# Kernel tuning notes

Measured on AMD Instinct MI355X. Metric: run time of the kernel, lower is better.

## Reference

```python
import jax, jax.numpy as jnp
import numpy as np

B, T, D = 2, 2048, 2048
NH, HD, R = 16, 128, 64
CQ, CKV = 1536, 512
WINDOW, CHUNK = 512, 256
MIN_SCALE, MAX_SCALE = 0.5, 2.0
ROPE_BASE = 500000.0
EPS = 1e-6


def setup_inputs() -> dict:
    key = jax.random.key(0)
    ks = jax.random.split(key, 12)
    w = lambda k, shape: (jax.random.normal(k, shape, jnp.float32) * 0.02)
    return {
        "x": jax.random.normal(ks[0], (B, T, D), jnp.float32),
        "uncertainty": jax.random.uniform(ks[1], (B, T), jnp.float32),
        "Wq_down": w(ks[2], (D, CQ)),
        "q_norm_w": jnp.ones((CQ,), jnp.float32),
        "Wq_up": w(ks[3], (CQ, NH * HD)),
        "Wq_rope": w(ks[4], (CQ, NH * R)),
        "Wkv_down": w(ks[5], (D, CKV)),
        "kv_norm_w": jnp.ones((CKV,), jnp.float32),
        "Wk_up": w(ks[6], (CKV, NH * HD)),
        "Wv_up": w(ks[7], (CKV, NH * HD)),
        "Wk_rope": w(ks[8], (D, NH * R)),
        "Wout": w(ks[9], (NH * HD, D)),
        "Wgate": w(ks[10], (D, 1)),
        "bgate": jnp.zeros((1,), jnp.float32),
    }


def rms_norm(x, w):
    return x * jax.lax.rsqrt(jnp.mean(x * x, axis=-1, keepdims=True) + EPS) * w


def epe_cos_sin(positions, uncertainty):
    # freq_idx = arange(r//2)*2/r ; theta = base**(-freq_idx)
    half = R // 2
    freq_idx = jnp.arange(half, dtype=jnp.float32) * 2.0 / R
    theta = ROPE_BASE ** (-freq_idx)                                  # [half]
    scale = MIN_SCALE + jnp.clip(uncertainty, 0.0, 1.0) * (MAX_SCALE - MIN_SCALE)  # [B,T]
    freqs = positions[None, :, None].astype(jnp.float32) * theta[None, None, :] * scale[:, :, None]
    freqs = freqs[:, :, None, :]                                      # [B,T,1,half]
    return jnp.cos(freqs), jnp.sin(freqs)


def apply_rope(x, cos, sin):
    # x: [B,T,nH,r]; rotate halves with per-(B,T) cos/sin broadcast over heads
    half = x.shape[-1] // 2
    x1, x2 = x[..., :half], x[..., half:]
    return jnp.concatenate([x1 * cos - x2 * sin, x2 * cos + x1 * sin], axis=-1)


def sliding_window_attn(Q, K, V, window, chunk):
    # Q,K: [B,nH,T,dk], V: [B,nH,T,dv]; chunked causal sliding-window
    b, nh, t, dk = Q.shape
    dv = V.shape[-1]
    half_w = window // 2
    n_chunks = t // chunk                    # T chosen multiple of chunk
    L = chunk + 2 * half_w
    Kp = jnp.pad(K, ((0, 0), (0, 0), (half_w, half_w), (0, 0)))
    Vp = jnp.pad(V, ((0, 0), (0, 0), (half_w, half_w), (0, 0)))
    starts = jnp.arange(n_chunks) * chunk
    idx = starts[:, None] + jnp.arange(L)[None, :]          # [nC,L] into padded axis
    Kw = Kp[:, :, idx]                                       # [B,nH,nC,L,dk]
    Vw = Vp[:, :, idx]                                       # [B,nH,nC,L,dv]
    Qc = Q.reshape(b, nh, n_chunks, chunk, dk)
    scores = jnp.einsum('bhcqd,bhckd->bhcqk', Qc, Kw) / jnp.sqrt(jnp.float32(dk))
    key_pos = idx - half_w                                   # actual key positions [nC,L]
    q_pos = starts[:, None] + jnp.arange(chunk)[None, :]     # [nC,chunk]
    mask = (key_pos[:, None, :] <= q_pos[:, :, None]) & (key_pos[:, None, :] >= 0)
    scores = jnp.where(mask[None, None], scores, -jnp.inf)
    p = jax.nn.softmax(scores, axis=-1)
    out = jnp.einsum('bhcqk,bhckd->bhcqd', p, Vw)
    return out.reshape(b, nh, t, dv)


def reference(x, uncertainty, Wq_down, q_norm_w, Wq_up, Wq_rope,
              Wkv_down, kv_norm_w, Wk_up, Wv_up, Wk_rope, Wout, Wgate, bgate):
    b, t, d = x.shape
    positions = jnp.arange(t)

    q_lat = rms_norm(x @ Wq_down, q_norm_w)                  # [B,T,CQ]
    q_c = (q_lat @ Wq_up).reshape(b, t, NH, HD)
    q_r = (q_lat @ Wq_rope).reshape(b, t, NH, R)
    kv_lat = rms_norm(x @ Wkv_down, kv_norm_w)               # [B,T,CKV]
    k_c = (kv_lat @ Wk_up).reshape(b, t, NH, HD)
    v = (kv_lat @ Wv_up).reshape(b, t, NH, HD)
    k_r = (x @ Wk_rope).reshape(b, t, NH, R)

    cos, sin = epe_cos_sin(positions, uncertainty)
    q_r = apply_rope(q_r, cos, sin)
    k_r = apply_rope(k_r, cos, sin)

    Q = jnp.concatenate([q_c, q_r], axis=-1).transpose(0, 2, 1, 3)   # [B,nH,T,HD+R]
    K = jnp.concatenate([k_c, k_r], axis=-1).transpose(0, 2, 1, 3)
    V = v.transpose(0, 2, 1, 3)                                       # [B,nH,T,HD]

    out_ar = sliding_window_attn(Q, K, V, WINDOW, CHUNK)

    # full bidirectional SDPA
    scale = 1.0 / jnp.sqrt(jnp.float32(HD + R))
    scores = jnp.einsum('bhqd,bhkd->bhqk', Q, K) * scale
    out_bidir = jnp.einsum('bhqk,bhkd->bhqd', jax.nn.softmax(scores, axis=-1), V)

    alpha = jax.nn.sigmoid((x @ Wgate + bgate)).squeeze(-1)           # [B,T]
    a = alpha[:, None, :, None]
    merged = a * out_bidir + (1.0 - a) * out_ar                       # [B,nH,T,HD]
    merged = merged.transpose(0, 2, 1, 3).reshape(b, t, NH * HD)
    return merged @ Wout, alpha
```

## Files before the change

kernel.cpp:

```cpp
#include <hip/hip_runtime.h>
#include <hip/hip_bf16.h>
#include <math.h>

typedef __hip_bfloat16 bf16;
using v8bf = __attribute__((ext_vector_type(8))) __bf16;
using v4f  = __attribute__((ext_vector_type(4))) float;
using f32x16 = __attribute__((ext_vector_type(16))) float;
using v4u = __attribute__((ext_vector_type(4))) unsigned;
using v4s = __attribute__((ext_vector_type(4))) short;
using v8s = __attribute__((ext_vector_type(8))) short;

#define T_SEQ 2048
#define DMODEL 2048
#define NHEADS 16
#define HDIM 128
#define RDIM 64

__device__ __forceinline__ short f2bfbits(float f) {
  bf16 h = __float2bfloat16(f);
  short s;
  __builtin_memcpy(&s, &h, 2);
  return s;
}

__device__ __forceinline__ float bfbits2f(short s) {
  bf16 h;
  __builtin_memcpy(&h, &s, 2);
  return __bfloat162float(h);
}

__device__ __forceinline__ unsigned pk2bf(float a, float b) {
  unsigned lo = (unsigned short)f2bfbits(a);
  unsigned hi = (unsigned short)f2bfbits(b);
  return lo | (hi << 16);
}

typedef const __attribute__((address_space(1))) unsigned gu32;
typedef __attribute__((address_space(3))) unsigned lu32;
__device__ __forceinline__ void gl_lds16(const void* g, void* l) {
  __builtin_amdgcn_global_load_lds((gu32*)g, (lu32*)l, 16, 0, 0);
}

__global__ void detect_k(const unsigned* __restrict__ x, int* __restrict__ flag) {
  __shared__ int cnt;
  if (threadIdx.x == 0) cnt = 0;
  __syncthreads();
  int c = 0;
#pragma unroll
  for (int i = 0; i < 4; i++) {
    unsigned w = x[threadIdx.x * 4 + i];
    unsigned e = (w >> 7) & 0xFFu;
    if (e < 97u || e > 157u) c++;
  }
  atomicAdd(&cnt, c);
  __syncthreads();
  if (threadIdx.x == 0) flag[0] = (cnt > 256) ? 1 : 0;
}

__global__ __launch_bounds__(256) void conv_all(const void* x_raw,
                                                const void* qnw_raw, const void* kvnw_raw,
                                                const void* wg_raw, const void* bg_raw,
                                                const void* unc_raw,
                                                bf16* xc, bf16* qnw, bf16* kvnw,
                                                bf16* wgc, bf16* bgc, float* uncf,
                                                const int* flag) {
  bool isf = (*flag != 0);
  if (blockIdx.x < 32768) {
    int i = blockIdx.x * 256 + threadIdx.x;
    xc[i] = isf ? __float2bfloat16(((const float*)x_raw)[i]) : ((const bf16*)x_raw)[i];
  } else {
    int i = (blockIdx.x - 32768) * 256 + threadIdx.x;
    if (i < 1536) qnw[i] = isf ? __float2bfloat16(((const float*)qnw_raw)[i]) : ((const bf16*)qnw_raw)[i];
    else if (i < 2048) { int j = i - 1536; kvnw[j] = isf ? __float2bfloat16(((const float*)kvnw_raw)[j]) : ((const bf16*)kvnw_raw)[j]; }
    else if (i < 4096) { int j = i - 2048; wgc[j] = isf ? __float2bfloat16(((const float*)wg_raw)[j]) : ((const bf16*)wg_raw)[j]; }
    else if (i < 4097) bgc[0] = isf ? __float2bfloat16(((const float*)bg_raw)[0]) : ((const bf16*)bg_raw)[0];
    else if (i < 8193) { int j = i - 4097; uncf[j] = isf ? ((const float*)unc_raw)[j] : __bfloat162float(((const bf16*)unc_raw)[j]); }
  }
}

struct TP8 {
  const void* s[8];
  bf16* d[8];
  int rows[8];
  int cols[8];
  int pre[9];
};

__global__ __launch_bounds__(256) void transpose_all(TP8 jobs, const int* __restrict__ flag) {
  __shared__ bf16 tile[32][33];
  int bid = blockIdx.x;
  int w = 0;
#pragma unroll
  for (int k = 0; k < 7; k++) if (bid >= jobs.pre[k + 1]) w = k + 1;
  int lt = bid - jobs.pre[w];
  int rows = jobs.rows[w], cols = jobs.cols[w];
  int tpr = cols >> 5;
  int by = (lt / tpr) << 5, bx = (lt % tpr) << 5;
  const void* src = jobs.s[w];
  bf16* dst = jobs.d[w];
  int tx = threadIdx.x & 31, ty = threadIdx.x >> 5;
  bool isf = (*flag != 0);
#pragma unroll
  for (int i = 0; i < 32; i += 8) {
    size_t idx = (size_t)(by + ty + i) * cols + bx + tx;
    tile[ty + i][tx] = isf ? __float2bfloat16(((const float*)src)[idx])
                           : ((const bf16*)src)[idx];
  }
  __syncthreads();
#pragma unroll
  for (int i = 0; i < 32; i += 8)
    dst[(size_t)(bx + ty + i) * rows + by + tx] = tile[tx][ty + i];
}

__global__ __launch_bounds__(256) void transpose_str(const bf16* __restrict__ src,
                                                     bf16* __restrict__ dst,
                                                     int srcStride, int dstStride) {
  __shared__ bf16 tile[32][33];
  int bx = blockIdx.x * 32, by = blockIdx.y * 32;
  int tx = threadIdx.x & 31, ty = threadIdx.x >> 5;
#pragma unroll
  for (int i = 0; i < 32; i += 8)
    tile[ty + i][tx] = src[(size_t)(by + ty + i) * srcStride + bx + tx];
  __syncthreads();
#pragma unroll
  for (int i = 0; i < 32; i += 8)
    dst[(size_t)(bx + ty + i) * dstStride + by + tx] = tile[tx][ty + i];
}

__global__ __launch_bounds__(256) void gemm_tn(const bf16* __restrict__ A,
                                               const bf16* __restrict__ BT,
                                               bf16* __restrict__ Cb,
                                               int M, int N, int K,
                                               const int* __restrict__ oflag,
                                               void* __restrict__ dvout) {
  __shared__ __align__(16) short lsa[128 * 32];
  __shared__ __align__(16) short lsb[128 * 32];
  const int m0 = blockIdx.y * 128, n0 = blockIdx.x * 128;
  const int tid = threadIdx.x;
  const int w = tid >> 6, lane = tid & 63, quad = lane >> 4, l16 = lane & 15;
  const int wm = (w >> 1) * 64, wn = (w & 1) * 64;
  const int srow = ((lane >> 5) & 1) * 8 + (lane & 7);
  const int skq  = (lane >> 3) & 3;
  const int r0 = w * 2, r1 = w * 2 + 1;
  const bf16* Ab0 = A  + (size_t)(m0 + r0 * 16 + srow) * K + skq * 8;
  const bf16* Ab1 = A  + (size_t)(m0 + r1 * 16 + srow) * K + skq * 8;
  const bf16* Bb0 = BT + (size_t)(n0 + r0 * 16 + srow) * K + skq * 8;
  const bf16* Bb1 = BT + (size_t)(n0 + r1 * 16 + srow) * K + skq * 8;
  short* la0 = &lsa[r0 * 512];
  short* la1 = &lsa[r1 * 512];
  short* lb0 = &lsb[r0 * 512];
  short* lb1 = &lsb[r1 * 512];

  v4f acc[4][4];
#pragma unroll
  for (int i = 0; i < 4; i++)
#pragma unroll
    for (int j = 0; j < 4; j++) acc[i][j] = (v4f){0.f, 0.f, 0.f, 0.f};

  for (int kb = 0; kb < K; kb += 32) {
    __syncthreads();
    gl_lds16(Ab0 + kb, la0);
    gl_lds16(Ab1 + kb, la1);
    gl_lds16(Bb0 + kb, lb0);
    gl_lds16(Bb1 + kb, lb1);
    __syncthreads();

    v8bf af[4], bfr[4];
#pragma unroll
    for (int i = 0; i < 4; i++) {
      int row = wm + i * 16 + l16;
      af[i] = *reinterpret_cast<const v8bf*>(
          &lsa[((row >> 3) << 8) + (quad << 6) + ((row & 7) << 3)]);
    }
#pragma unroll
    for (int j = 0; j < 4; j++) {
      int row = wn + j * 16 + l16;
      bfr[j] = *reinterpret_cast<const v8bf*>(
          &lsb[((row >> 3) << 8) + (quad << 6) + ((row & 7) << 3)]);
    }
#pragma unroll
    for (int i = 0; i < 4; i++)
#pragma unroll
      for (int j = 0; j < 4; j++)
        acc[i][j] = __builtin_amdgcn_mfma_f32_16x16x32_bf16(af[i], bfr[j], acc[i][j], 0, 0, 0);
  }
  const bool isf = dvout && (*oflag != 0);
#pragma unroll
  for (int i = 0; i < 4; i++)
#pragma unroll
    for (int j = 0; j < 4; j++)
#pragma unroll
      for (int r = 0; r < 4; r++) {
        int row = m0 + wm + i * 16 + quad * 4 + r;
        int col = n0 + wn + j * 16 + l16;
        float vv = acc[i][j][r];
        size_t idx = (size_t)row * N + col;
        if (dvout) {
          if (isf) ((float*)dvout)[idx] = vv;
          else     ((bf16*)dvout)[idx] = __float2bfloat16(vv);
        } else {
          Cb[idx] = __float2bfloat16(vv);
        }
      }
}

__global__ __launch_bounds__(256) void rmsnorm_both(const bf16* __restrict__ xproj,
                                                    const bf16* __restrict__ qnw,
                                                    const bf16* __restrict__ kvnw,
                                                    bf16* __restrict__ q_lat,
                                                    bf16* __restrict__ kv_lat) {
  int bid = blockIdx.x, tid = threadIdx.x;
  bool isq = bid < 4096;
  int row = isq ? bid : bid - 4096;
  int C = isq ? 1536 : 512;
  const bf16* r = xproj + (size_t)row * 3072 + (isq ? 0 : 1536);
  const bf16* w = isq ? qnw : kvnw;
  bf16* o = (isq ? q_lat : kv_lat) + (size_t)row * C;
  float s = 0.f;
  for (int i = tid; i < C; i += 256) { float v = __bfloat162float(r[i]); s += v * v; }
#pragma unroll
  for (int m = 32; m; m >>= 1) s += __shfl_xor(s, m);
  __shared__ float red[4];
  if ((tid & 63) == 0) red[tid >> 6] = s;
  __syncthreads();
  float tot = red[0] + red[1] + red[2] + red[3];
  float rs = rsqrtf(tot / (float)C + 1e-6f);
  for (int i = tid; i < C; i += 256)
    o[i] = __float2bfloat16(__bfloat162float(r[i]) * rs * __bfloat162float(w[i]));
}

__global__ __launch_bounds__(256) void rope_gate(bf16* __restrict__ qcr,
                                                 bf16* __restrict__ xproj,
                                                 const float* __restrict__ unc,
                                                 const bf16* __restrict__ x,
                                                 const bf16* __restrict__ wg,
                                                 const bf16* __restrict__ bg,
                                                 float* __restrict__ af,
                                                 void* __restrict__ dout,
                                                 const int* __restrict__ flag) {
  __shared__ float red[4];
  int tid = threadIdx.x;
  if (blockIdx.x < 8192) {
    int idx = blockIdx.x * 256 + tid;
    int j = idx & 31, h = (idx >> 5) & 15, bt = idx >> 9;
    int t = bt & (T_SEQ - 1);
    float u = unc[bt];
    u = fminf(fmaxf(u, 0.f), 1.f);
    float scale = 0.5f + 1.5f * u;
    float theta = expf(-(float)j * (1.f / 32.f) * logf(500000.f));
    float f = (float)t * theta * scale;
    float c = cosf(f), s = sinf(f);
    size_t base = (size_t)bt * 3072 + 2048 + h * RDIM + j;
    {
      float x1 = __bfloat162float(qcr[base]), x2 = __bfloat162float(qcr[base + 32]);
      qcr[base]      = __float2bfloat16(x1 * c - x2 * s);
      qcr[base + 32] = __float2bfloat16(x2 * c + x1 * s);
    }
    {
      float x1 = __bfloat162float(xproj[base]), x2 = __bfloat162float(xproj[base + 32]);
      xproj[base]      = __float2bfloat16(x1 * c - x2 * s);
      xproj[base + 32] = __float2bfloat16(x2 * c + x1 * s);
    }
  } else {
    int row = blockIdx.x - 8192;
    const bf16* xr = x + (size_t)row * DMODEL;
    float s = 0.f;
    for (int i = tid; i < DMODEL; i += 256)
      s += __bfloat162float(xr[i]) * __bfloat162float(wg[i]);
#pragma unroll
    for (int m = 32; m; m >>= 1) s += __shfl_xor(s, m);
    if ((tid & 63) == 0) red[tid >> 6] = s;
    __syncthreads();
    if (tid == 0) {
      float tot = red[0] + red[1] + red[2] + red[3] + __bfloat162float(bg[0]);
      float a = 1.f / (1.f + expf(-tot));
      af[row] = a;
      size_t oi = (size_t)8388608 + row;
      if (*flag) ((float*)dout)[oi] = a;
      else       ((bf16*)dout)[oi] = __float2bfloat16(a);
    }
  }
}

template <int IS_AR>
__global__ __launch_bounds__(256, 2) void attn_k(const bf16* __restrict__ qcr,
                                                 const bf16* __restrict__ kcv,
                                                 const bf16* __restrict__ xproj,
                                                 const bf16* __restrict__ vt,
                                                 const bf16* __restrict__ ob,
                                                 const float* __restrict__ alphaF,
                                                 bf16* __restrict__ out) {
  constexpr int LDK = 200;
  constexpr int LDV = 72;
  __shared__ __align__(16) short sh[64 * LDK + 128 * LDV];
  short* lk  = sh;
  short* lvt = sh + 64 * LDK;

  const int b = blockIdx.z, h = blockIdx.y, qt = blockIdx.x;
  const int qs = qt * 128;
  const int tid = threadIdx.x;
  const int w = tid >> 6, lane = tid & 63;
  const int l5 = lane & 31, h8 = lane >> 5;
  const int q0 = qs + w * 32;
  const int myq = q0 + l5;

  v8bf qf[12];
  {
    const bf16* qcb = qcr + ((size_t)b * T_SEQ + myq) * 3072 + h * HDIM;
#pragma unroll
    for (int ks = 0; ks < 8; ks++)
      qf[ks] = *reinterpret_cast<const v8bf*>(qcb + ks * 16 + h8 * 8);
    const bf16* qrb = qcr + ((size_t)b * T_SEQ + myq) * 3072 + 2048 + h * RDIM;
#pragma unroll
    for (int ks = 0; ks < 4; ks++)
      qf[8 + ks] = *reinterpret_cast<const v8bf*>(qrb + ks * 16 + h8 * 8);
  }

  float l_sum = 0.f;
  f32x16 oacc[4];
#pragma unroll
  for (int nd = 0; nd < 4; nd++)
#pragma unroll
    for (int r = 0; r < 16; r++) oacc[nd][r] = 0.f;

  int klo = 0, khi = T_SEQ;
  if (IS_AR) {
    int c = qs >> 8;
    klo = (c > 0) ? (c * 256 - 256) : 0;
    khi = qs + 128;
  }
  const float sc = 0.07216878364870323f;

  for (int kb = klo; kb < khi; kb += 64) {
    __syncthreads();
#pragma unroll
    for (int i = 0; i < 6; i++) {
      int c = i * 256 + tid;
      int row = c / 24, dg = c - row * 24;
      int key = kb + row;
      const bf16* src = (dg < 16)
          ? kcv + ((size_t)b * T_SEQ + key) * 4096 + h * HDIM + dg * 8
          : xproj + ((size_t)b * T_SEQ + key) * 3072 + 2048 + h * RDIM + (dg - 16) * 8;
      *reinterpret_cast<v8bf*>(&lk[row * LDK + dg * 8]) = *reinterpret_cast<const v8bf*>(src);
    }
#pragma unroll
    for (int i = 0; i < 4; i++) {
      int c = i * 256 + tid;
      int d = c >> 3, kg = c & 7;
      *reinterpret_cast<v8bf*>(&lvt[d * LDV + kg * 8]) =
          *reinterpret_cast<const v8bf*>(vt + (size_t)(h * HDIM + d) * (2 * T_SEQ) + b * T_SEQ + kb + kg * 8);
    }
    __syncthreads();

    if (IS_AR && kb > q0 + 31) continue;

    __builtin_amdgcn_s_setprio(1);
    v8bf pfrag[4];
#pragma unroll
    for (int j = 0; j < 2; j++) {
      bool jact = !IS_AR || (kb + j * 32 <= q0 + 31);
      if (jact) {
        f32x16 s;
#pragma unroll
        for (int r = 0; r < 16; r++) s[r] = 0.f;
#pragma unroll
        for (int ks = 0; ks < 12; ks++) {
          v8bf kf = *reinterpret_cast<const v8bf*>(&lk[(j * 32 + l5) * LDK + ks * 16 + h8 * 8]);
          s = __builtin_amdgcn_mfma_f32_32x32x16_bf16(kf, qf[ks], s, 0, 0, 0);
        }
        float p[16];
#pragma unroll
        for (int r = 0; r < 16; r++) {
          float e = __expf(s[r] * sc);
          if (IS_AR) {
            int k = kb + j * 32 + (r & 3) + 8 * (r >> 2) + 4 * h8;
            e = (k <= myq) ? e : 0.f;
          }
          p[r] = e;
          l_sum += e;
        }
#pragma unroll
        for (int cc = 0; cc < 2; cc++) {
          unsigned Y0 = pk2bf(p[cc * 8 + 0], p[cc * 8 + 1]);
          unsigned Y1 = pk2bf(p[cc * 8 + 2], p[cc * 8 + 3]);
          unsigned Y2 = pk2bf(p[cc * 8 + 4], p[cc * 8 + 5]);
          unsigned Y3 = pk2bf(p[cc * 8 + 6], p[cc * 8 + 7]);
          asm volatile("v_permlane32_swap_b32 %0, %1" : "+v"(Y0), "+v"(Y2));
          asm volatile("v_permlane32_swap_b32 %0, %1" : "+v"(Y1), "+v"(Y3));
          v4u t; t.x = Y0; t.y = Y1; t.z = Y2; t.w = Y3;
          pfrag[j * 2 + cc] = __builtin_bit_cast(v8bf, t);
        }
      } else {
#pragma unroll
        for (int cc = 0; cc < 2; cc++) {
          v4u t; t.x = 0; t.y = 0; t.z = 0; t.w = 0;
          pfrag[j * 2 + cc] = __builtin_bit_cast(v8bf, t);
        }
      }
    }
#pragma unroll
    for (int ck = 0; ck < 4; ck++) {
#pragma unroll
      for (int nd = 0; nd < 4; nd++) {
        v8bf vf = *reinterpret_cast<const v8bf*>(&lvt[(nd * 32 + l5) * LDV + ck * 16 + h8 * 8]);
        oacc[nd] = __builtin_amdgcn_mfma_f32_32x32x16_bf16(vf, pfrag[ck], oacc[nd], 0, 0, 0);
      }
    }
    __builtin_amdgcn_s_setprio(0);
  }

  l_sum += __shfl_xor(l_sum, 32);
  float inv = 1.f / l_sum;

  __syncthreads();
  short* tile = sh + w * (32 * 136);
#pragma unroll
  for (int nd = 0; nd < 4; nd++)
#pragma unroll
    for (int rg = 0; rg < 4; rg++) {
      v4s pk;
#pragma unroll
      for (int i = 0; i < 4; i++) pk[i] = f2bfbits(oacc[nd][rg * 4 + i] * inv);
      *reinterpret_cast<v4s*>(&tile[l5 * 136 + nd * 32 + rg * 8 + h8 * 4]) = pk;
    }
  __syncthreads();
#pragma unroll
  for (int i = 0; i < 8; i++) {
    int r = i * 4 + (lane >> 4);
    int q2 = q0 + r;
    int dcol = (lane & 15) * 8;
    v8s mv = *reinterpret_cast<const v8s*>(&tile[r * 136 + dcol]);
    size_t gbase = ((size_t)b * T_SEQ + q2) * DMODEL + h * HDIM + dcol;
    if (IS_AR) {
      float a = alphaF[b * T_SEQ + q2];
      v8s ov = *reinterpret_cast<const v8s*>((const void*)(ob + gbase));
      v8s res;
#pragma unroll
      for (int e = 0; e < 8; e++)
        res[e] = f2bfbits(a * bfbits2f(ov[e]) + (1.f - a) * bfbits2f(mv[e]));
      *reinterpret_cast<v8s*>((void*)(out + gbase)) = res;
    } else {
      *reinterpret_cast<v8s*>((void*)(out + gbase)) = mv;
    }
  }
}

extern "C" void kernel_launch(void* const* d_in, const int* in_sizes, int n_in,
                              void* d_out, int out_size, void* d_ws, size_t ws_size,
                              hipStream_t stream) {
  const void* x_raw    = d_in[0];
  const void* unc_raw  = d_in[1];
  const void* Wqd_raw  = d_in[2];
  const void* qnw_raw  = d_in[3];
  const void* Wqu_raw  = d_in[4];
  const void* Wqr_raw  = d_in[5];
  const void* Wkvd_raw = d_in[6];
  const void* kvnw_raw = d_in[7];
  const void* Wku_raw  = d_in[8];
  const void* Wvu_raw  = d_in[9];
  const void* Wkr_raw  = d_in[10];
  const void* Wo_raw   = d_in[11];
  const void* Wg_raw   = d_in[12];
  const void* bg_raw   = d_in[13];

  char* ws = (char*)d_ws;
  size_t off = 0;
  auto alloc = [&](size_t bytes) -> void* {
    char* p = ws + off;
    off += (bytes + 255) & ~(size_t)255;
    return p;
  };
  int*  flag   = (int*)alloc(256);
  bf16* xc     = (bf16*)alloc((size_t)4096 * 2048 * 2);
  float* uncf  = (float*)alloc((size_t)4096 * 4);
  bf16* qnw    = (bf16*)alloc(1536 * 2);
  bf16* kvnw   = (bf16*)alloc(512 * 2);
  bf16* wgc    = (bf16*)alloc(2048 * 2);
  bf16* bgc    = (bf16*)alloc(256);
  bf16* BT1    = (bf16*)alloc((size_t)3072 * 2048 * 2);
  bf16* BT2    = (bf16*)alloc((size_t)3072 * 1536 * 2);
  bf16* BT3    = (bf16*)alloc((size_t)4096 * 512 * 2);
  bf16* WoT    = (bf16*)alloc((size_t)2048 * 2048 * 2);
  bf16* xproj  = (bf16*)alloc((size_t)4096 * 3072 * 2);
  bf16* q_lat  = (bf16*)alloc((size_t)4096 * 1536 * 2);
  bf16* kv_lat = (bf16*)alloc((size_t)4096 * 512 * 2);
  bf16* qcr    = (bf16*)alloc((size_t)4096 * 3072 * 2);
  bf16* kcv    = (bf16*)alloc((size_t)4096 * 4096 * 2);
  bf16* vT     = (bf16*)alloc((size_t)4096 * 2048 * 2);
  bf16* out_b  = (bf16*)alloc((size_t)4096 * 2048 * 2);
  bf16* attno  = (bf16*)alloc((size_t)4096 * 2048 * 2);
  float* alphaF= (float*)alloc((size_t)4096 * 4);

  detect_k<<<1, 256, 0, stream>>>((const unsigned*)x_raw, flag);

  conv_all<<<32801, 256, 0, stream>>>(x_raw, qnw_raw, kvnw_raw, Wg_raw, bg_raw, unc_raw,
                                      xc, qnw, kvnw, wgc, bgc, uncf, flag);

  TP8 jobs;
  const void* srcs[8] = {Wqd_raw, Wkvd_raw, Wkr_raw, Wqu_raw, Wqr_raw, Wku_raw, Wvu_raw, Wo_raw};
  bf16* dsts[8] = {BT1, BT1 + (size_t)1536 * 2048, BT1 + (size_t)2048 * 2048,
                   BT2, BT2 + (size_t)2048 * 1536,
                   BT3, BT3 + (size_t)2048 * 512, WoT};
  int rws[8] = {2048, 2048, 2048, 1536, 1536, 512, 512, 2048};
  int cls[8] = {1536, 512, 1024, 2048, 1024, 2048, 2048, 2048};
  int acc_t = 0;
  for (int i = 0; i < 8; i++) {
    jobs.s[i] = srcs[i]; jobs.d[i] = dsts[i];
    jobs.rows[i] = rws[i]; jobs.cols[i] = cls[i];
    jobs.pre[i] = acc_t;
    acc_t += (rws[i] / 32) * (cls[i] / 32);
  }
  jobs.pre[8] = acc_t;
  transpose_all<<<acc_t, 256, 0, stream>>>(jobs, flag);

  auto gemmb = [&](const bf16* A, const bf16* BT, bf16* C, int M, int N, int K) {
    gemm_tn<<<dim3(N / 128, M / 128), 256, 0, stream>>>(A, BT, C, M, N, K, nullptr, nullptr);
  };

  gemmb(xc, BT1, xproj, 4096, 3072, 2048);
  rmsnorm_both<<<8192, 256, 0, stream>>>(xproj, qnw, kvnw, q_lat, kv_lat);
  gemmb(q_lat, BT2, qcr, 4096, 3072, 1536);
  gemmb(kv_lat, BT3, kcv, 4096, 4096, 512);

  transpose_str<<<dim3(64, 128), 256, 0, stream>>>(kcv + 2048, vT, 4096, 4096);

  rope_gate<<<12288, 256, 0, stream>>>(qcr, xproj, uncf, xc, wgc, bgc, alphaF, d_out, flag);

  attn_k<0><<<dim3(16, 16, 2), 256, 0, stream>>>(qcr, kcv, xproj, vT, nullptr, nullptr, out_b);
  attn_k<1><<<dim3(16, 16, 2), 256, 0, stream>>>(qcr, kcv, xproj, vT, out_b, alphaF, attno);

  gemm_tn<<<dim3(16, 32), 256, 0, stream>>>(attno, WoT, nullptr, 4096, 2048, 2048, flag, d_out);

  (void)in_sizes; (void)n_in; (void)out_size; (void)ws_size;
}
```

Before: 674.8 us.

## Fuse sliding-window and bidirectional attention into one pass with register prefetch

Replaces the two attention kernel launches (bidirectional, then sliding-window with blend) with one kernel. It reorders key blocks so the windowed causal range is visited first, snapshots the partial sums at the diagonal block as the sliding-window output, then carries on to finish the full softmax. The alpha blend is folded into the normalisation. Next-tile K/V global loads are also issued into registers before compute, to overlap memory with MFMA work. In exchange, the AR partial goes through a strided fp32 scratch buffer and register pressure rises.

Measured after the change: 679.3 us. No clear change (+0.7%).

```diff
diff --git a/kernel.cpp b/kernel.cpp
--- a/kernel.cpp
+++ b/kernel.cpp
@@ -282,13 +282,12 @@
   }
 }
 
-template <int IS_AR>
-__global__ __launch_bounds__(256, 2) void attn_k(const bf16* __restrict__ qcr,
+__global__ __launch_bounds__(256, 2) void attn_f(const bf16* __restrict__ qcr,
                                                  const bf16* __restrict__ kcv,
                                                  const bf16* __restrict__ xproj,
                                                  const bf16* __restrict__ vt,
-                                                 const bf16* __restrict__ ob,
                                                  const float* __restrict__ alphaF,
+                                                 float* __restrict__ arp,
                                                  bf16* __restrict__ out) {
   constexpr int LDK = 200;
   constexpr int LDV = 72;
@@ -323,125 +322,185 @@
 #pragma unroll
     for (int r = 0; r < 16; r++) oacc[nd][r] = 0.f;
 
-  int klo = 0, khi = T_SEQ;
-  if (IS_AR) {
-    int c = qs >> 8;
-    klo = (c > 0) ? (c * 256 - 256) : 0;
-    khi = qs + 128;
-  }
+  const float a_q = alphaF[b * T_SEQ + myq];
   const float sc = 0.07216878364870323f;
 
-  for (int kb = klo; kb < khi; kb += 64) {
+  const int c   = qs >> 8;
+  const int klo = (c > 0) ? (c * 256 - 256) : 0;
+  const int A   = klo >> 6;
+  const int n1  = ((qs + 128) >> 6) - A;
+  const int diag_idx = n1 - 2 + (w >> 1);
+
+  int koc[4], ldc_[4];
+#pragma unroll
+  for (int i = 0; i < 4; i++) {
+    int cc = i * 256 + tid;
+    int row = cc >> 4, dg = cc & 15;
+    koc[i]  = row * 4096 + dg * 8;
+    ldc_[i] = row * LDK + dg * 8;
+  }
+  int kor[2], ldr_[2];
+#pragma unroll
+  for (int i = 0; i < 2; i++) {
+    int cc = i * 256 + tid;
+    int row = cc >> 3, dg = cc & 7;
+    kor[i]  = row * 3072 + dg * 8;
+    ldr_[i] = row * LDK + 128 + dg * 8;
+  }
+  int kov[4], ldv_[4];
+#pragma unroll
+  for (int i = 0; i < 4; i++) {
+    int cc = i * 256 + tid;
+    int d = cc >> 3, kg = cc & 7;
+    kov[i]  = d * 4096 + kg * 8;
+    ldv_[i] = d * LDV + kg * 8;
+  }
+  const bf16* kc_base = kcv   + (size_t)b * T_SEQ * 4096 + h * HDIM;
+  const bf16* kr_base = xproj + (size_t)b * T_SEQ * 3072 + 2048 + h * RDIM;
+  const bf16* v_base  = vt    + (size_t)h * HDIM * (2 * T_SEQ) + b * T_SEQ;
+
+  v4u rc[4], rr[2], rv[4];
+  auto kb_of = [&](int idx) -> int {
+    int t = (idx < n1) ? (A + idx) : ((idx < n1 + A) ? (idx - n1) : idx);
+    return t << 6;
+  };
+  auto issue = [&](int kb) {
+    const bf16* pc = kc_base + (size_t)kb * 4096;
+    const bf16* pr = kr_base + (size_t)kb * 3072;
+    const bf16* pv = v_base + kb;
+#pragma unroll
+    for (int i = 0; i < 4; i++) rc[i] = *reinterpret_cast<const v4u*>(pc + koc[i]);
+#pragma unroll
+    for (int i = 0; i < 2; i++) rr[i] = *reinterpret_cast<const v4u*>(pr + kor[i]);
+#pragma unroll
+    for (int i = 0; i < 4; i++) rv[i] = *reinterpret_cast<const v4u*>(pv + kov[i]);
+  };
+
+  auto qk = [&](int j) -> f32x16 {
+    f32x16 s;
+#pragma unroll
+    for (int r = 0; r < 16; r++) s[r] = 0.f;
+#pragma unroll
+    for (int ks = 0; ks < 12; ks++) {
+      v8bf kf = *reinterpret_cast<const v8bf*>(&lk[(j * 32 + l5) * LDK + ks * 16 + h8 * 8]);
+      s = __builtin_amdgcn_mfma_f32_32x32x16_bf16(kf, qf[ks], s, 0, 0, 0);
+    }
+    return s;
+  };
+  auto packf = [&](const float* p, v8bf* pf) {
+#pragma unroll
+    for (int cc = 0; cc < 2; cc++) {
+      unsigned Y0 = pk2bf(p[cc * 8 + 0], p[cc * 8 + 1]);
+      unsigned Y1 = pk2bf(p[cc * 8 + 2], p[cc * 8 + 3]);
+      unsigned Y2 = pk2bf(p[cc * 8 + 4], p[cc * 8 + 5]);
+      unsigned Y3 = pk2bf(p[cc * 8 + 6], p[cc * 8 + 7]);
+      asm volatile("v_permlane32_swap_b32 %0, %1" : "+v"(Y0), "+v"(Y2));
+      asm volatile("v_permlane32_swap_b32 %0, %1" : "+v"(Y1), "+v"(Y3));
+      v4u t; t.x = Y0; t.y = Y1; t.z = Y2; t.w = Y3;
+      pf[cc] = __builtin_bit_cast(v8bf, t);
+    }
+  };
+  auto pvj = [&](int j, const v8bf* pf) {
+#pragma unroll
+    for (int ck = 0; ck < 2; ck++)
+#pragma unroll
+      for (int nd = 0; nd < 4; nd++) {
+        v8bf vf = *reinterpret_cast<const v8bf*>(&lvt[(nd * 32 + l5) * LDV + (j * 2 + ck) * 16 + h8 * 8]);
+        oacc[nd] = __builtin_amdgcn_mfma_f32_32x32x16_bf16(vf, pf[ck], oacc[nd], 0, 0, 0);
+      }
+  };
+  auto plainpass = [&](const f32x16& s, int j) {
+    float p[16];
+#pragma unroll
+    for (int r = 0; r < 16; r++) { float e = __expf(s[r] * sc); p[r] = e; l_sum += e; }
+    v8bf pf[2];
+    packf(p, pf);
+    pvj(j, pf);
+  };
+  auto maskpass = [&](const f32x16& s, int j, int kb, bool upper) {
+    float p[16];
+#pragma unroll
+    for (int r = 0; r < 16; r++) {
+      int kk = kb + j * 32 + (r & 3) + 8 * (r >> 2) + 4 * h8;
+      float e = __expf(s[r] * sc);
+      bool keep = upper ? (kk > myq) : (kk <= myq);
+      e = keep ? e : 0.f;
+      p[r] = e;
+      l_sum += e;
+    }
+    v8bf pf[2];
+    packf(p, pf);
+    pvj(j, pf);
+  };
+
+  issue(kb_of(0));
+
+  for (int idx = 0; idx < 32; idx++) {
+    const int kb = kb_of(idx);
     __syncthreads();
 #pragma unroll
-    for (int i = 0; i < 6; i++) {
-      int c = i * 256 + tid;
-      int row = c / 24, dg = c - row * 24;
-      int key = kb + row;
-      const bf16* src = (dg < 16)
-          ? kcv + ((size_t)b * T_SEQ + key) * 4096 + h * HDIM + dg * 8
-          : xproj + ((size_t)b * T_SEQ + key) * 3072 + 2048 + h * RDIM + (dg - 16) * 8;
-      *reinterpret_cast<v8bf*>(&lk[row * LDK + dg * 8]) = *reinterpret_cast<const v8bf*>(src);
-    }
-#pragma unroll
-    for (int i = 0; i < 4; i++) {
-      int c = i * 256 + tid;
-      int d = c >> 3, kg = c & 7;
-      *reinterpret_cast<v8bf*>(&lvt[d * LDV + kg * 8]) =
-          *reinterpret_cast<const v8bf*>(vt + (size_t)(h * HDIM + d) * (2 * T_SEQ) + b * T_SEQ + kb + kg * 8);
-    }
+    for (int i = 0; i < 4; i++) *reinterpret_cast<v4u*>(&lk[ldc_[i]]) = rc[i];
+#pragma unroll
+    for (int i = 0; i < 2; i++) *reinterpret_cast<v4u*>(&lk[ldr_[i]]) = rr[i];
+#pragma unroll
+    for (int i = 0; i < 4; i++) *reinterpret_cast<v4u*>(&lvt[ldv_[i]]) = rv[i];
+    if (idx + 1 < 32) issue(kb_of(idx + 1));
     __syncthreads();
 
-    if (IS_AR && kb > q0 + 31) continue;
-
     __builtin_amdgcn_s_setprio(1);
-    v8bf pfrag[4];
-#pragma unroll
-    for (int j = 0; j < 2; j++) {
-      bool jact = !IS_AR || (kb + j * 32 <= q0 + 31);
-      if (jact) {
-        f32x16 s;
-#pragma unroll
-        for (int r = 0; r < 16; r++) s[r] = 0.f;
-#pragma unroll
-        for (int ks = 0; ks < 12; ks++) {
-          v8bf kf = *reinterpret_cast<const v8bf*>(&lk[(j * 32 + l5) * LDK + ks * 16 + h8 * 8]);
-          s = __builtin_amdgcn_mfma_f32_32x32x16_bf16(kf, qf[ks], s, 0, 0, 0);
-        }
-        float p[16];
-#pragma unroll
-        for (int r = 0; r < 16; r++) {
-          float e = __expf(s[r] * sc);
-          if (IS_AR) {
-            int k = kb + j * 32 + (r & 3) + 8 * (r >> 2) + 4 * h8;
-            e = (k <= myq) ? e : 0.f;
+    if (idx != diag_idx) {
+      plainpass(qk(0), 0);
+      plainpass(qk(1), 1);
+    } else {
+      f32x16 s0 = qk(0);
+      f32x16 s1 = qk(1);
+      maskpass(s0, 0, kb, false);
+      maskpass(s1, 1, kb, false);
+      {
+        float lar = l_sum + __shfl_xor(l_sum, 32);
+        float invar = (1.f - a_q) / lar;
+#pragma unroll
+        for (int nd = 0; nd < 4; nd++)
+#pragma unroll
+          for (int r = 0; r < 16; r++) {
+            int d = nd * 32 + (r & 3) + 8 * (r >> 2) + 4 * h8;
+            arp[((size_t)((b * NHEADS + h) * HDIM + d)) * T_SEQ + myq] = oacc[nd][r] * invar;
           }
-          p[r] = e;
-          l_sum += e;
-        }
-#pragma unroll
-        for (int cc = 0; cc < 2; cc++) {
-          unsigned Y0 = pk2bf(p[cc * 8 + 0], p[cc * 8 + 1]);
-          unsigned Y1 = pk2bf(p[cc * 8 + 2], p[cc * 8 + 3]);
-          unsigned Y2 = pk2bf(p[cc * 8 + 4], p[cc * 8 + 5]);
-          unsigned Y3 = pk2bf(p[cc * 8 + 6], p[cc * 8 + 7]);
-          asm volatile("v_permlane32_swap_b32 %0, %1" : "+v"(Y0), "+v"(Y2));
-          asm volatile("v_permlane32_swap_b32 %0, %1" : "+v"(Y1), "+v"(Y3));
-          v4u t; t.x = Y0; t.y = Y1; t.z = Y2; t.w = Y3;
-          pfrag[j * 2 + cc] = __builtin_bit_cast(v8bf, t);
-        }
-      } else {
-#pragma unroll
-        for (int cc = 0; cc < 2; cc++) {
-          v4u t; t.x = 0; t.y = 0; t.z = 0; t.w = 0;
-          pfrag[j * 2 + cc] = __builtin_bit_cast(v8bf, t);
-        }
       }
-    }
-#pragma unroll
-    for (int ck = 0; ck < 4; ck++) {
-#pragma unroll
-      for (int nd = 0; nd < 4; nd++) {
-        v8bf vf = *reinterpret_cast<const v8bf*>(&lvt[(nd * 32 + l5) * LDV + ck * 16 + h8 * 8]);
-        oacc[nd] = __builtin_amdgcn_mfma_f32_32x32x16_bf16(vf, pfrag[ck], oacc[nd], 0, 0, 0);
-      }
+      maskpass(s0, 0, kb, true);
+      maskpass(s1, 1, kb, true);
     }
     __builtin_amdgcn_s_setprio(0);
   }
 
   l_sum += __shfl_xor(l_sum, 32);
-  float inv = 1.f / l_sum;
+  float inv = a_q / l_sum;
 
   __syncthreads();
   short* tile = sh + w * (32 * 136);
+  const float* arpb = arp + (size_t)((b * NHEADS + h) * HDIM) * T_SEQ + myq;
 #pragma unroll
   for (int nd = 0; nd < 4; nd++)
 #pragma unroll
     for (int rg = 0; rg < 4; rg++) {
       v4s pk;
 #pragma unroll
-      for (int i = 0; i < 4; i++) pk[i] = f2bfbits(oacc[nd][rg * 4 + i] * inv);
+      for (int i = 0; i < 4; i++) {
+        int d = nd * 32 + rg * 8 + h8 * 4 + i;
+        float val = oacc[nd][rg * 4 + i] * inv + arpb[(size_t)d * T_SEQ];
+        pk[i] = f2bfbits(val);
+      }
       *reinterpret_cast<v4s*>(&tile[l5 * 136 + nd * 32 + rg * 8 + h8 * 4]) = pk;
     }
   __syncthreads();
 #pragma unroll
   for (int i = 0; i < 8; i++) {
     int r = i * 4 + (lane >> 4);
-    int q2 = q0 + r;
+    int q2 = qs + w * 32 + r;
     int dcol = (lane & 15) * 8;
     v8s mv = *reinterpret_cast<const v8s*>(&tile[r * 136 + dcol]);
     size_t gbase = ((size_t)b * T_SEQ + q2) * DMODEL + h * HDIM + dcol;
-    if (IS_AR) {
-      float a = alphaF[b * T_SEQ + q2];
-      v8s ov = *reinterpret_cast<const v8s*>((const void*)(ob + gbase));
-      v8s res;
-#pragma unroll
-      for (int e = 0; e < 8; e++)
-        res[e] = f2bfbits(a * bfbits2f(ov[e]) + (1.f - a) * bfbits2f(mv[e]));
-      *reinterpret_cast<v8s*>((void*)(out + gbase)) = res;
-    } else {
-      *reinterpret_cast<v8s*>((void*)(out + gbase)) = mv;
-    }
+    *reinterpret_cast<v8s*>((void*)(out + gbase)) = mv;
   }
 }
 
@@ -487,7 +546,7 @@
   bf16* qcr    = (bf16*)alloc((size_t)4096 * 3072 * 2);
   bf16* kcv    = (bf16*)alloc((size_t)4096 * 4096 * 2);
   bf16* vT     = (bf16*)alloc((size_t)4096 * 2048 * 2);
-  bf16* out_b  = (bf16*)alloc((size_t)4096 * 2048 * 2);
+  float* arp   = (float*)alloc((size_t)2 * NHEADS * HDIM * T_SEQ * 4);
   bf16* attno  = (bf16*)alloc((size_t)4096 * 2048 * 2);
   float* alphaF= (float*)alloc((size_t)4096 * 4);
 
@@ -526,8 +585,7 @@
 
   rope_gate<<<12288, 256, 0, stream>>>(qcr, xproj, uncf, xc, wgc, bgc, alphaF, d_out, flag);
 
-  attn_k<0><<<dim3(16, 16, 2), 256, 0, stream>>>(qcr, kcv, xproj, vT, nullptr, nullptr, out_b);
-  attn_k<1><<<dim3(16, 16, 2), 256, 0, stream>>>(qcr, kcv, xproj, vT, out_b, alphaF, attno);
+  attn_f<<<dim3(16, 16, 2), 256, 0, stream>>>(qcr, kcv, xproj, vT, alphaF, arp, attno);
 
   gemm_tn<<<dim3(16, 32), 256, 0, stream>>>(attno, WoT, nullptr, 4096, 2048, 2048, flag, d_out);
 
```
